# Optimization experiments

Hardware: AMD Instinct MI355X
Metric: run time of the kernel (lower is better)

The kernel has to match this reference:

```python
import jax, jax.numpy as jnp
import numpy as np

K = 3
KK = K * K


def _offset_mask_conv(x, ow, ob):
    # Conv2d(C_in, 3*KK, k=3, stride=1, pad=1) in NCHW/OIHW
    y = jax.lax.conv_general_dilated(
        x, ow, window_strides=(1, 1), padding=((1, 1), (1, 1)),
        dimension_numbers=('NCHW', 'OIHW', 'NCHW'))
    return y + ob[None, :, None, None]


def _bilinear(xb, gy, gx):
    # xb: [C,H,W]; gy,gx: [KK,H,W] pixel coords (align_corners=True => pixel==unnormalized)
    # padding_mode='zeros': out-of-range taps contribute 0.
    C, H, W = xb.shape
    x0f = jnp.floor(gx); y0f = jnp.floor(gy)
    x0 = x0f.astype(jnp.int32); y0 = y0f.astype(jnp.int32)
    x1 = x0 + 1; y1 = y0 + 1
    wx1 = gx - x0f; wy1 = gy - y0f
    wx0 = 1.0 - wx1; wy0 = 1.0 - wy1

    def gather(yi, xi):
        valid = (yi >= 0) & (yi < H) & (xi >= 0) & (xi < W)
        yc = jnp.clip(yi, 0, H - 1)
        xc = jnp.clip(xi, 0, W - 1)
        v = xb[:, yc, xc]  # [C,KK,H,W]
        return v * valid[None].astype(xb.dtype)

    return (gather(y0, x0) * (wy0 * wx0)[None]
            + gather(y0, x1) * (wy0 * wx1)[None]
            + gather(y1, x0) * (wy1 * wx0)[None]
            + gather(y1, x1) * (wy1 * wx1)[None])  # [C,KK,H,W]


def setup_inputs() -> dict:
    key = jax.random.key(0)
    k1, k2, k3, k4 = jax.random.split(key, 4)
    B, C, Cout, H, W = 8, 64, 64, 128, 128
    x = jax.random.normal(k1, (B, C, H, W), dtype=jnp.float32)
    # offset/mask conv params (small, so offsets stay in a realistic range)
    ow = jax.random.normal(k2, (3 * KK, C, K, K), dtype=jnp.float32) * 0.01
    ob = jnp.zeros((3 * KK,), dtype=jnp.float32)
    # main conv weight (kaiming-ish scale) and bias
    w = jax.random.normal(k3, (Cout, C, K, K), dtype=jnp.float32) * (1.0 / np.sqrt(C * KK))
    b = jax.random.normal(k4, (Cout,), dtype=jnp.float32) * 0.01
    return {"x": x, "ow": ow, "ob": ob, "w": w, "b": b}


def reference(x, ow, ob, w, b):
    B, C, H, W = x.shape
    om = _offset_mask_conv(x, ow, ob)            # [B, 3*KK, H, W]
    off_x = om[:, :KK]                           # o1 -> x-offset
    off_y = om[:, KK:2 * KK]                     # o2 -> y-offset
    mask = jax.nn.sigmoid(om[:, 2 * KK:])        # [B,KK,H,W]

    gh, gw = jnp.meshgrid(jnp.arange(H, dtype=x.dtype), jnp.arange(W, dtype=x.dtype), indexing='ij')
    d = jnp.arange(-(K // 2), K // 2 + 1, dtype=x.dtype)
    kh, kw = jnp.meshgrid(d, d, indexing='ij')
    dh = kh.reshape(-1)                          # [KK] row-major (dh,dw) order matches weight[...,i,j]
    dw = kw.reshape(-1)

    gx = gw[None, None] + dw[None, :, None, None] + off_x   # [B,KK,H,W]
    gy = gh[None, None] + dh[None, :, None, None] + off_y

    sampled = jax.vmap(_bilinear)(x, gy, gx)     # [B,C,KK,H,W]
    sampled = sampled * mask[:, None]            # modulation

    wflat = w.reshape(w.shape[0], w.shape[1], KK)  # [Cout,C,KK]
    out = jnp.einsum('bckhw,ock->bohw', sampled, wflat) + b[None, :, None, None]
    return out
```

## Files before the change

kernel.cpp:

```cpp
#include <hip/hip_runtime.h>

#define B 8
#define C 64
#define H 128
#define W 128
#define HW (H * W)
#define OC 27
#define KK 9
#define COUT 64
#define KDIM 576
#define LDSROW 1152
#define NPIX 16
#define NPAIR (NPIX * KK)

typedef __attribute__((ext_vector_type(8))) short s16x8;
typedef __attribute__((ext_vector_type(4))) float f32x4;

__device__ inline ushort f2bf(float f) {
    union { float f; unsigned u; } uv;
    uv.f = f;
    unsigned r = uv.u + 0x7FFF + ((uv.u >> 16) & 1);
    return (ushort)(r >> 16);
}
__device__ inline float bf2f(ushort u) {
    return __uint_as_float((unsigned)u << 16);
}

__global__ __launch_bounds__(256) void k_transpose_x(const float* __restrict__ x,
                                                     ushort* __restrict__ xTb) {
    __shared__ float lds[64][65];
    int j = blockIdx.x;
    int vb = (j & 7) * 256 + (j >> 3);
    int b = vb >> 8;
    int tile = vb & 255;
    int hw0 = tile * 64;
    int lane = threadIdx.x & 63;
    int cg = threadIdx.x >> 6;
#pragma unroll
    for (int r = 0; r < 16; ++r) {
        int c = cg * 16 + r;
        lds[c][lane] = x[(size_t)(b * C + c) * HW + hw0 + lane];
    }
    __syncthreads();
#pragma unroll
    for (int r = 0; r < 16; ++r) {
        int hwl = cg * 16 + r;
        xTb[(size_t)(b * HW + hw0 + hwl) * C + lane] = f2bf(lds[lane][hwl]);
    }
}

__global__ __launch_bounds__(256) void k_prep_w(const float* __restrict__ w,
                                                ushort* __restrict__ wB) {
    int idx = blockIdx.x * 256 + threadIdx.x;
    if (idx >= COUT * KDIM) return;
    int o = idx / KDIM;
    int Kx = idx % KDIM;
    int k = Kx >> 6;
    int c = Kx & 63;
    wB[idx] = f2bf(w[(size_t)(o * C + c) * KK + k]);
}

__global__ __launch_bounds__(256) void k_prep_aw(const float* __restrict__ ow,
                                                 ushort* __restrict__ awB) {
    int idx = blockIdx.x * 256 + threadIdx.x;
    if (idx >= 32 * KDIM) return;
    int o = idx / KDIM;
    int Kx = idx % KDIM;
    int tap = Kx >> 6;
    int c = Kx & 63;
    float v = (o < OC) ? ow[((size_t)o * C + c) * KK + tap] : 0.0f;
    awB[idx] = f2bf(v);
}

__global__ __launch_bounds__(256) void k_om(const ushort* __restrict__ xTb,
                                            const ushort* __restrict__ awB,
                                            const float* __restrict__ ob,
                                            float4* __restrict__ gW,
                                            int2* __restrict__ gO) {
    __shared__ __align__(16) char xwin[3 * 66 * 128];
    int tid = threadIdx.x;
    int lane = tid & 63;
    int wv = tid >> 6;
    int j = blockIdx.x;
    int vb = (j & 7) * 256 + (j >> 3);
    int b = vb >> 8;
    int h = (vb >> 1) & 127;
    int w0 = (vb & 1) * 64;

    const ushort* xb = xTb + (size_t)b * (HW * C);
    int ch2 = tid & 31;
#pragma unroll
    for (int it = 0; it < 25; ++it) {
        int pi = it * 8 + (tid >> 5);
        if (pi < 198) {
            int row = pi / 66;
            int col = pi - row * 66;
            int y = h - 1 + row;
            int xc = w0 - 1 + col;
            unsigned v = 0;
            if ((unsigned)y < H && (unsigned)xc < W)
                v = *(const unsigned*)(xb + ((size_t)(y * W + xc) << 6) + ch2 * 2);
            int byte = (pi * 128 + ch2 * 4) ^ ((col & 7) << 4);
            *(unsigned*)(xwin + byte) = v;
        }
    }
    __syncthreads();

    f32x4 acc0 = {0.f, 0.f, 0.f, 0.f};
    f32x4 acc1 = {0.f, 0.f, 0.f, 0.f};
    int pixl = lane & 15;
    int q = lane >> 4;
    int base_col = wv * 16 + pixl;
    const ushort* a0 = awB + (size_t)pixl * KDIM + q * 8;
    const ushort* a1 = awB + (size_t)(16 + pixl) * KDIM + q * 8;
#pragma unroll
    for (int s = 0; s < 18; ++s) {
        int tap = s >> 1;
        int row = tap / 3;
        int cs = tap - row * 3;
        int col = base_col + cs;
        int c0b = ((s & 1) * 32 + q * 8) * 2;
        int byte = (((row * 66 + col) << 7) + c0b) ^ ((col & 7) << 4);
        s16x8 bfrag = *(const s16x8*)(xwin + byte);
        s16x8 af0 = *(const s16x8*)(a0 + s * 32);
        s16x8 af1 = *(const s16x8*)(a1 + s * 32);
        acc0 = __builtin_amdgcn_mfma_f32_16x16x32_bf16(af0, bfrag, acc0, 0, 0, 0);
        acc1 = __builtin_amdgcn_mfma_f32_16x16x32_bf16(af1, bfrag, acc1, 0, 0, 0);
    }

    __syncthreads();
    float* omt = (float*)xwin;
    {
        int pix = wv * 16 + pixl;
#pragma unroll
        for (int jj = 0; jj < 4; ++jj) {
            int oc = q * 4 + jj;
            omt[pix * 29 + oc] = acc0[jj] + ob[oc];
        }
#pragma unroll
        for (int jj = 0; jj < 4; ++jj) {
            int oc1 = 16 + q * 4 + jj;
            if (oc1 < OC) omt[pix * 29 + oc1] = acc1[jj] + ob[oc1];
        }
    }
    __syncthreads();

    size_t base9 = ((size_t)b * HW + h * W + w0) * KK;
    for (int t = tid; t < 64 * KK; t += 256) {
        int pix = t / 9;
        int k = t - pix * 9;
        float offx = omt[pix * 29 + k];
        float offy = omt[pix * 29 + 9 + k];
        float mlog = omt[pix * 29 + 18 + k];
        int dh = k / 3 - 1;
        int dw = k % 3 - 1;
        float mask = 1.0f / (1.0f + __expf(-mlog));
        float gx = (float)(w0 + pix + dw) + offx;
        float gy = (float)(h + dh) + offy;
        float x0f = floorf(gx), y0f = floorf(gy);
        int x0 = (int)x0f, y0 = (int)y0f;
        int x1 = x0 + 1, y1 = y0 + 1;
        float wx1 = gx - x0f, wy1 = gy - y0f;
        float wx0 = 1.0f - wx1, wy0 = 1.0f - wy1;
        float rw0 = ((unsigned)y0 < H) ? wy0 * mask : 0.0f;
        float rw1 = ((unsigned)y1 < H) ? wy1 * mask : 0.0f;
        int y0c = min(max(y0, 0), H - 1), y1c = min(max(y1, 0), H - 1);
        int colbase = min(max(x0, 0), W - 2);
        float cw0 = 0.0f, cw1 = 0.0f;
        if ((unsigned)x0 < W) { if (x0 == colbase) cw0 += wx0; else cw1 += wx0; }
        if ((unsigned)x1 < W) { if (x1 == colbase) cw0 += wx1; else cw1 += wx1; }
        gW[base9 + t] = make_float4(rw0 * cw0, rw0 * cw1, rw1 * cw0, rw1 * cw1);
        gO[base9 + t] = make_int2((y0c * W + colbase) * (C * 2),
                                  (y1c * W + colbase) * (C * 2));
    }
}

__global__ __launch_bounds__(256, 5) void k_main(const ushort* __restrict__ xTb,
                                                 const float4* __restrict__ gW,
                                                 const int2* __restrict__ gO,
                                                 const ushort* __restrict__ wB,
                                                 const float* __restrict__ bias,
                                                 float* __restrict__ out) {
    __shared__ __align__(16) char smem[NPIX * LDSROW];
    __shared__ float4 mw_lds[NPAIR];
    __shared__ int2 mo_lds[NPAIR];

    int tid = threadIdx.x;
    int lane = tid & 63;
    int wv = tid >> 6;
    int jb = blockIdx.x;
    int vb = (jb & 7) * 1024 + (jb >> 3);
    int pb = vb * NPIX;
    int b = pb >> 14;
    int rem = pb & (HW - 1);
    int h = rem >> 7;
    int w0 = rem & (W - 1);

    size_t base9 = ((size_t)b * HW + rem) * KK;
    if (tid < NPAIR) mw_lds[tid] = gW[base9 + tid];
    if (tid < NPAIR) mo_lds[tid] = gO[base9 + tid];
    __syncthreads();

    const char* xbase = (const char*)(xTb + (size_t)b * (HW * C));
    bool lo_half = lane < 32;
#pragma unroll 1
    for (int pp = 0; pp < 4; ++pp) {
        int p = wv * 4 + pp;
        float4 mwv[KK];
        int2 mov[KK];
#pragma unroll
        for (int k = 0; k < KK; ++k) {
            mwv[k] = mw_lds[p * 9 + k];
            mov[k] = mo_lds[p * 9 + k];
        }
        unsigned d0[KK], d1[KK];
#pragma unroll
        for (int k = 0; k < KK; ++k) {
            d0[k] = *(const unsigned*)(xbase + mov[k].x + lane * 4);
            d1[k] = *(const unsigned*)(xbase + mov[k].y + lane * 4);
        }
        __builtin_amdgcn_sched_barrier(0);
        int vlds = p * LDSROW + (((lane & 31) * 4) ^ ((p & 7) << 4));
#pragma unroll
        for (int k = 0; k < KK; ++k) {
            float wa = lo_half ? mwv[k].x : mwv[k].y;
            float wb_ = lo_half ? mwv[k].z : mwv[k].w;
            float a0 = __uint_as_float(d0[k] << 16);
            float a1 = __uint_as_float(d0[k] & 0xFFFF0000u);
            float b0 = __uint_as_float(d1[k] << 16);
            float b1 = __uint_as_float(d1[k] & 0xFFFF0000u);
            float p0 = a0 * wa + b0 * wb_;
            float p1 = a1 * wa + b1 * wb_;
            float q0 = __shfl_xor(p0, 32, 64);
            float q1 = __shfl_xor(p1, 32, 64);
            float s0 = p0 + q0, s1 = p1 + q1;
            unsigned pk;
            asm("v_cvt_pk_bf16_f32 %0, %1, %2" : "=v"(pk) : "v"(s0), "v"(s1));
            if (lane < 32) *(unsigned*)(smem + vlds + k * 128) = pk;
        }
    }
    __syncthreads();

    f32x4 acc;
#pragma unroll
    for (int j = 0; j < 4; ++j) acc[j] = bias[wv * 16 + (lane >> 4) * 4 + j];

    int pix = lane & 15;
    const ushort* wrow = wB + (size_t)(wv * 16 + pix) * KDIM + (lane >> 4) * 8;
#pragma unroll
    for (int s = 0; s < 18; ++s) {
        int kbyte = s * 64 + (lane >> 4) * 16;
        int byte = (pix * LDSROW + kbyte) ^ ((pix & 7) << 4);
        s16x8 bfrag = *(const s16x8*)(smem + byte);
        s16x8 afrag = *(const s16x8*)(wrow + s * 32);
        acc = __builtin_amdgcn_mfma_f32_16x16x32_bf16(afrag, bfrag, acc, 0, 0, 0);
    }

    float* obase = out + ((size_t)(b * COUT + wv * 16 + (lane >> 4) * 4) * HW) + h * W + w0;
#pragma unroll
    for (int j = 0; j < 4; ++j) obase[(size_t)j * HW + pix] = acc[j];
}

extern "C" void kernel_launch(void* const* d_in, const int* in_sizes, int n_in,
                              void* d_out, int out_size, void* d_ws, size_t ws_size,
                              hipStream_t stream) {
    const float* x = (const float*)d_in[0];
    const float* ow = (const float*)d_in[1];
    const float* ob = (const float*)d_in[2];
    const float* w = (const float*)d_in[3];
    const float* bias = (const float*)d_in[4];
    float* out = (float*)d_out;

    float4* gW = (float4*)d_ws;
    int2* gO = (int2*)(gW + (size_t)B * HW * KK);
    ushort* xTb = (ushort*)(gO + (size_t)B * HW * KK);
    ushort* wB = xTb + (size_t)B * HW * C;
    ushort* awB = wB + (size_t)COUT * KDIM;

    hipLaunchKernelGGL(k_transpose_x, dim3(B * 256), dim3(256), 0, stream, x, xTb);
    hipLaunchKernelGGL(k_prep_w, dim3((COUT * KDIM + 255) / 256), dim3(256), 0,
                       stream, w, wB);
    hipLaunchKernelGGL(k_prep_aw, dim3((32 * KDIM + 255) / 256), dim3(256), 0,
                       stream, ow, awB);
    hipLaunchKernelGGL(k_om, dim3(B * H * 2), dim3(256), 0, stream, xTb, awB, ob, gW, gO);
    hipLaunchKernelGGL(k_main, dim3(B * HW / NPIX), dim3(256), 0, stream,
                       xTb, gW, gO, wB, bias, out);
}
```

Baseline: 162.8 us.

## Move bilinear metadata computation into main kernel and double pixels per block

```diff
diff --git a/kernel.cpp b/kernel.cpp
--- a/kernel.cpp
+++ b/kernel.cpp
@@ -10,8 +10,8 @@
 #define COUT 64
 #define KDIM 576
 #define LDSROW 1152
-#define NPIX 16
-#define NPAIR (NPIX * KK)
+#define NPIX 32
+#define NMETA (NPIX * KK)
 
 typedef __attribute__((ext_vector_type(8))) short s16x8;
 typedef __attribute__((ext_vector_type(4))) float f32x4;
@@ -75,8 +75,7 @@
 __global__ __launch_bounds__(256) void k_om(const ushort* __restrict__ xTb,
                                             const ushort* __restrict__ awB,
                                             const float* __restrict__ ob,
-                                            float4* __restrict__ gW,
-                                            int2* __restrict__ gO) {
+                                            float* __restrict__ om_pm) {
     __shared__ __align__(16) char xwin[3 * 66 * 128];
     int tid = threadIdx.x;
     int lane = tid & 63;
@@ -145,13 +144,43 @@
     }
     __syncthreads();
 
-    size_t base9 = ((size_t)b * HW + h * W + w0) * KK;
-    for (int t = tid; t < 64 * KK; t += 256) {
-        int pix = t / 9;
-        int k = t - pix * 9;
-        float offx = omt[pix * 29 + k];
-        float offy = omt[pix * 29 + 9 + k];
-        float mlog = omt[pix * 29 + 18 + k];
+    float* dst = om_pm + ((size_t)b * HW + h * W + w0) * 32;
+#pragma unroll
+    for (int t = tid; t < 64 * 32; t += 256) {
+        int pix = t >> 5;
+        int oc = t & 31;
+        float v = (oc < OC) ? omt[pix * 29 + oc] : 0.0f;
+        dst[(size_t)pix * 32 + oc] = v;
+    }
+}
+
+__global__ __launch_bounds__(512) void k_main(const ushort* __restrict__ xTb,
+                                              const float* __restrict__ om_pm,
+                                              const ushort* __restrict__ wB,
+                                              const float* __restrict__ bias,
+                                              float* __restrict__ out) {
+    __shared__ __align__(16) char smem[NPIX * LDSROW];
+    __shared__ float4 mw_lds[NMETA];
+    __shared__ int2 mo_lds[NMETA];
+
+    int tid = threadIdx.x;
+    int lane = tid & 63;
+    int wv = tid >> 6;
+    int jb = blockIdx.x;
+    int vb = (jb & 7) * 512 + (jb >> 3);
+    int pb = vb * NPIX;
+    int b = pb >> 14;
+    int rem = pb & (HW - 1);
+    int h = rem >> 7;
+    int w0 = rem & (W - 1);
+
+    if (tid < NMETA) {
+        int pix = tid / 9;
+        int k = tid - pix * 9;
+        const float* o0 = om_pm + ((size_t)b * HW + rem + pix) * 32;
+        float offx = o0[k];
+        float offy = o0[9 + k];
+        float mlog = o0[18 + k];
         int dh = k / 3 - 1;
         int dw = k % 3 - 1;
         float mask = 1.0f / (1.0f + __expf(-mlog));
@@ -169,36 +198,10 @@
         float cw0 = 0.0f, cw1 = 0.0f;
         if ((unsigned)x0 < W) { if (x0 == colbase) cw0 += wx0; else cw1 += wx0; }
         if ((unsigned)x1 < W) { if (x1 == colbase) cw0 += wx1; else cw1 += wx1; }
-        gW[base9 + t] = make_float4(rw0 * cw0, rw0 * cw1, rw1 * cw0, rw1 * cw1);
-        gO[base9 + t] = make_int2((y0c * W + colbase) * (C * 2),
-                                  (y1c * W + colbase) * (C * 2));
-    }
-}
-
-__global__ __launch_bounds__(256, 5) void k_main(const ushort* __restrict__ xTb,
-                                                 const float4* __restrict__ gW,
-                                                 const int2* __restrict__ gO,
-                                                 const ushort* __restrict__ wB,
-                                                 const float* __restrict__ bias,
-                                                 float* __restrict__ out) {
-    __shared__ __align__(16) char smem[NPIX * LDSROW];
-    __shared__ float4 mw_lds[NPAIR];
-    __shared__ int2 mo_lds[NPAIR];
-
-    int tid = threadIdx.x;
-    int lane = tid & 63;
-    int wv = tid >> 6;
-    int jb = blockIdx.x;
-    int vb = (jb & 7) * 1024 + (jb >> 3);
-    int pb = vb * NPIX;
-    int b = pb >> 14;
-    int rem = pb & (HW - 1);
-    int h = rem >> 7;
-    int w0 = rem & (W - 1);
-
-    size_t base9 = ((size_t)b * HW + rem) * KK;
-    if (tid < NPAIR) mw_lds[tid] = gW[base9 + tid];
-    if (tid < NPAIR) mo_lds[tid] = gO[base9 + tid];
+        mw_lds[tid] = make_float4(rw0 * cw0, rw0 * cw1, rw1 * cw0, rw1 * cw1);
+        mo_lds[tid] = make_int2((y0c * W + colbase) * (C * 2),
+                                (y1c * W + colbase) * (C * 2));
+    }
     __syncthreads();
 
     const char* xbase = (const char*)(xTb + (size_t)b * (HW * C));
@@ -241,24 +244,26 @@
     }
     __syncthreads();
 
+    int mrow = (wv & 3) * 16;
+    int pixsel = ((wv >> 2) << 4) + (lane & 15);
     f32x4 acc;
 #pragma unroll
-    for (int j = 0; j < 4; ++j) acc[j] = bias[wv * 16 + (lane >> 4) * 4 + j];
-
-    int pix = lane & 15;
-    const ushort* wrow = wB + (size_t)(wv * 16 + pix) * KDIM + (lane >> 4) * 8;
+    for (int j = 0; j < 4; ++j) acc[j] = bias[mrow + (lane >> 4) * 4 + j];
+
+    const ushort* wrow = wB + (size_t)(mrow + (lane & 15)) * KDIM + (lane >> 4) * 8;
 #pragma unroll
     for (int s = 0; s < 18; ++s) {
         int kbyte = s * 64 + (lane >> 4) * 16;
-        int byte = (pix * LDSROW + kbyte) ^ ((pix & 7) << 4);
+        int byte = (pixsel * LDSROW + kbyte) ^ ((pixsel & 7) << 4);
         s16x8 bfrag = *(const s16x8*)(smem + byte);
         s16x8 afrag = *(const s16x8*)(wrow + s * 32);
         acc = __builtin_amdgcn_mfma_f32_16x16x32_bf16(afrag, bfrag, acc, 0, 0, 0);
     }
 
-    float* obase = out + ((size_t)(b * COUT + wv * 16 + (lane >> 4) * 4) * HW) + h * W + w0;
-#pragma unroll
-    for (int j = 0; j < 4; ++j) obase[(size_t)j * HW + pix] = acc[j];
+    float* obase = out + ((size_t)(b * COUT + mrow + (lane >> 4) * 4) * HW) + h * W +
+                   w0 + ((wv >> 2) << 4);
+#pragma unroll
+    for (int j = 0; j < 4; ++j) obase[(size_t)j * HW + (lane & 15)] = acc[j];
 }
 
 extern "C" void kernel_launch(void* const* d_in, const int* in_sizes, int n_in,
@@ -271,9 +276,8 @@
     const float* bias = (const float*)d_in[4];
     float* out = (float*)d_out;
 
-    float4* gW = (float4*)d_ws;
-    int2* gO = (int2*)(gW + (size_t)B * HW * KK);
-    ushort* xTb = (ushort*)(gO + (size_t)B * HW * KK);
+    float* om_pm = (float*)d_ws;
+    ushort* xTb = (ushort*)(om_pm + (size_t)B * HW * 32);
     ushort* wB = xTb + (size_t)B * HW * C;
     ushort* awB = wB + (size_t)COUT * KDIM;
 
@@ -282,7 +286,7 @@
                        stream, w, wB);
     hipLaunchKernelGGL(k_prep_aw, dim3((32 * KDIM + 255) / 256), dim3(256), 0,
                        stream, ow, awB);
-    hipLaunchKernelGGL(k_om, dim3(B * H * 2), dim3(256), 0, stream, xTb, awB, ob, gW, gO);
-    hipLaunchKernelGGL(k_main, dim3(B * HW / NPIX), dim3(256), 0, stream,
-                       xTb, gW, gO, wB, bias, out);
-}
+    hipLaunchKernelGGL(k_om, dim3(B * H * 2), dim3(256), 0, stream, xTb, awB, ob, om_pm);
+    hipLaunchKernelGGL(k_main, dim3(B * HW / NPIX), dim3(512), 0, stream,
+                       xTb, om_pm, wB, bias, out);
+}
```

Measured after the change: 180.2 us. 1.11x slower.
